# Performance work log

Measured on AMD Instinct MI355X. Metric: run time of the kernel, lower is better.

The kernel has to match this reference:

```python
import jax, jax.numpy as jnp
import numpy as np

LBASE = 256
L1_BASE = LBASE // 2 + 1   # 129
LPA = 128
L1_PA = LPA + 1            # 129
L2 = 16
L2_HALF = L2 // 2          # 8
L3 = 64
LOUTPUT = L3 + LPA + LBASE // 2  # 320
MAX_PLY = 60
COUNT = 6
BUCKET_SIZE = MAX_PLY // COUNT   # 10
B = 262144


def setup_inputs() -> dict:
    key = jax.random.key(0)
    ks = jax.random.split(key, 12)
    def w(k, shape, fan_in):
        bound = 1.0 / np.sqrt(fan_in)
        return jax.random.uniform(k, shape, jnp.float32, -bound, bound)
    return {
        "x_base": jax.random.uniform(ks[0], (B, LBASE // 2), jnp.float32),
        "x_pa": jax.random.uniform(ks[1], (B, LPA), jnp.float32),
        "mobility": jax.random.uniform(ks[2], (B, 1), jnp.float32),
        "ply": jax.random.randint(ks[3], (B,), 0, MAX_PLY),
        "W1b": w(ks[4], (COUNT, L2_HALF, L1_BASE), L1_BASE),
        "b1b": w(ks[5], (COUNT, L2_HALF), L1_BASE),
        "W1pa": w(ks[6], (COUNT, L2_HALF, L1_PA), L1_PA),
        "b1pa": w(ks[7], (COUNT, L2_HALF), L1_PA),
        "W2": w(ks[8], (COUNT, L3, L2 * 2), L2 * 2),
        "b2": w(ks[9], (COUNT, L3), L2 * 2),
        "Wout": w(ks[10], (COUNT, 1, LOUTPUT), LOUTPUT),
        "bout": jnp.zeros((COUNT, 1), jnp.float32),  # bias zeroed in __init__
    }


def _stacked_linear(x, W, b, idx):
    # per-sample bucket selection: x (B,I), W (C,O,I), b (C,O), idx (B,)
    return jnp.einsum("bi,boi->bo", x, W[idx]) + b[idx]


def reference(x_base, x_pa, mobility, ply, W1b, b1b, W1pa, b1pa, W2, b2, Wout, bout):
    idx = ply // BUCKET_SIZE                                   # (B,)
    mob = jnp.minimum(mobility * (7.0 / 255.0), 1.0)           # clamp max only
    xb = jnp.concatenate([x_base, mob], axis=1)                # (B,129)
    xpa = jnp.concatenate([x_pa, mob], axis=1)                 # (B,129)
    l1 = jnp.concatenate([
        _stacked_linear(xb, W1b, b1b, idx),
        _stacked_linear(xpa, W1pa, b1pa, idx),
    ], axis=1)                                                 # (B,16)
    l1_sq = jnp.square(l1) * (255.0 / 256.0)
    l1c = jnp.clip(jnp.concatenate([l1_sq, l1], axis=1), 0.0, 1.0)  # (B,32)
    l2x = _stacked_linear(l1c, W2, b2, idx)                    # (B,64)
    l2x = jnp.square(jnp.clip(l2x, 0.0, 1.0)) * (255.0 / 256.0)
    feats = jnp.concatenate([l2x, x_base, x_pa], axis=1)       # (B,320)
    return _stacked_linear(feats, Wout, bout, idx)             # (B,1)
```

## Files before the change

### kernel.cpp

```cpp
#include <hip/hip_runtime.h>


#define NB 6
#define BT 512
#define NW (BT / 64)

typedef _Float16 h2 __attribute__((ext_vector_type(2)));
typedef _Float16 h8 __attribute__((ext_vector_type(8)));
typedef float f4 __attribute__((ext_vector_type(4)));

__device__ __forceinline__ h2 pk2(float x, float y) {
    return __builtin_bit_cast(h2, __builtin_amdgcn_cvt_pkrtz(x, y));
}

__device__ __forceinline__ h8 pack8(const float4 a, const float4 b) {
    h2 p0 = pk2(a.x, a.y), p1 = pk2(a.z, a.w);
    h2 p2 = pk2(b.x, b.y), p3 = pk2(b.z, b.w);
    h8 r;
    r[0] = p0[0]; r[1] = p0[1]; r[2] = p1[0]; r[3] = p1[1];
    r[4] = p2[0]; r[5] = p2[1]; r[6] = p3[0]; r[7] = p3[1];
    return r;
}

__device__ __forceinline__ float actv(float v) {
    float u = fminf(fmaxf(v, 0.0f), 1.0f);
    return u * u * (255.0f / 256.0f);
}

__global__ __launch_bounds__(BT, 4)
void layerstacks_mfma(const float* __restrict__ x_base,
                      const float* __restrict__ x_pa,
                      const float* __restrict__ mobility,
                      const int*   __restrict__ ply,
                      const float* __restrict__ W1b,
                      const float* __restrict__ b1b,
                      const float* __restrict__ W1pa,
                      const float* __restrict__ b1pa,
                      const float* __restrict__ W2,
                      const float* __restrict__ b2,
                      const float* __restrict__ Wout,
                      const float* __restrict__ bout,
                      float* __restrict__ out)
{
    __shared__ __align__(16) _Float16 sW1[NB][2][4][4][9][8];
    __shared__ __align__(16) _Float16 sW2[NB][4][4][16][8];
    __shared__ float sWo0[NB][64];
    __shared__ float sB2[NB][64];
    __shared__ float sB1[NB][4][8];
    __shared__ float sBout[NB];
    __shared__ float sMob[BT];
    __shared__ int   sList[BT + NB * 16];
    __shared__ __align__(16) char sL1[NW * 1280];
    __shared__ int sCnt[8], sCur[8], sTb[40];
    __shared__ int sNt;

    const int tid   = threadIdx.x;
    const int lane  = tid & 63;
    const int w     = tid >> 6;
    const int gbase = blockIdx.x * BT;

    if (tid < 8) { sCnt[tid] = 0; }

    for (int e = tid; e < NB * 2 * 4 * 4 * 9 * 8; e += BT) {
        int i = e & 7;
        int rest = e >> 3;
        int n = rest % 9;   rest /= 9;
        int kb = rest & 3;  rest >>= 2;
        int t = rest & 3;   rest >>= 2;
        int st = rest & 1;
        int b = rest >> 1;
        int k = t * 32 + kb * 8 + i;
        float v;
        if (n < 8) {
            const float* Wx = st ? W1pa : W1b;
            v = Wx[b * 1032 + n * 129 + k];
        } else {
            v = st ? Wout[b * 320 + 192 + k] : Wout[b * 320 + 64 + k];
        }
        sW1[b][st][t][kb][n][i] = (_Float16)v;
    }
    for (int e = tid; e < NB * 4 * 4 * 16 * 8; e += BT) {
        int i = e & 7;
        int j = (e >> 3) & 15;
        int kb = (e >> 7) & 3;
        int T = (e >> 9) & 3;
        int b = e >> 11;
        int n = T * 16 + j;
        int k = kb * 8 + i;
        int u = k >> 1;
        int colw = (k & 1) ? (16 + u) : u;
        sW2[b][T][kb][j][i] = (_Float16)W2[b * 2048 + n * 32 + colw];
    }
    for (int e = tid; e < NB * 64; e += BT) {
        int b = e >> 6, n = e & 63;
        sWo0[b][n] = Wout[b * 320 + n];
        sB2[b][n]  = b2[e];
    }
    if (tid < NB * 4 * 8) {
        int n = tid & 7, which = (tid >> 3) & 3, b = tid >> 5;
        float v;
        if (which == 0)      v = b1b[b * 8 + n];
        else if (which == 1) v = b1pa[b * 8 + n];
        else if (which == 2) v = W1b [b * 1032 + n * 129 + 128];
        else                 v = W1pa[b * 1032 + n * 129 + 128];
        sB1[b][which][n] = v;
    }
    if (tid < NB) sBout[tid] = bout[tid];
    sMob[tid] = fminf(mobility[gbase + tid] * (7.0f / 255.0f), 1.0f);
    for (int e = tid; e < BT + NB * 16; e += BT) sList[e] = -1;

    const int bb = ply[gbase + tid] / 10;
    __syncthreads();

    #pragma unroll
    for (int b = 0; b < NB; ++b) {
        unsigned long long mk = __ballot(bb == b);
        if (bb == b) {
            int lead = __ffsll((long long)mk) - 1;
            if (lane == lead) atomicAdd(&sCnt[b], __popcll(mk));
        }
    }
    __syncthreads();

    if (tid == 0) {
        int off = 0, tt = 0;
        for (int b = 0; b < NB; ++b) {
            sCur[b] = off;
            int ntl = (sCnt[b] + 15) >> 4;
            for (int q = 0; q < ntl; ++q) sTb[tt++] = b;
            off += ntl << 4;
        }
        sNt = tt;
    }
    __syncthreads();

    #pragma unroll
    for (int b = 0; b < NB; ++b) {
        unsigned long long mk = __ballot(bb == b);
        if (bb == b) {
            int lead = __ffsll((long long)mk) - 1;
            int pfx = __popcll(mk & ((1ull << lane) - 1ull));
            int base = 0;
            if (lane == lead) base = atomicAdd(&sCur[b], __popcll(mk));
            base = __shfl(base, lead);
            sList[base + pfx] = tid;
        }
    }
    __syncthreads();

    const int ntiles = sNt;
    const int col = lane & 15;
    const int qd  = lane >> 4;
    char* lb = sL1 + w * 1280;

    for (int tl = w; tl < ntiles; tl += NW) {
        const int bkt = sTb[tl];
        const int t16 = tl << 4;

        const int sl0 = sList[t16 + qd * 4 + 0];
        const int sl1 = sList[t16 + qd * 4 + 1];
        const int sl2 = sList[t16 + qd * 4 + 2];
        const int sl3 = sList[t16 + qd * 4 + 3];
        int sA = sList[t16 + col];
        if (sA < 0) sA = sList[t16];

        const float* xbrow = x_base + (size_t)(gbase + sA) * 128 + qd * 8;
        const float* xprow = x_pa   + (size_t)(gbase + sA) * 128 + qd * 8;
        const float4 b00 = *(const float4*)(xbrow + 0);
        const float4 b01 = *(const float4*)(xbrow + 4);
        const float4 b10 = *(const float4*)(xbrow + 32);
        const float4 b11 = *(const float4*)(xbrow + 36);
        const float4 b20 = *(const float4*)(xbrow + 64);
        const float4 b21 = *(const float4*)(xbrow + 68);
        const float4 b30 = *(const float4*)(xbrow + 96);
        const float4 b31 = *(const float4*)(xbrow + 100);
        const float4 q00 = *(const float4*)(xprow + 0);
        const float4 q01 = *(const float4*)(xprow + 4);
        const float4 q10 = *(const float4*)(xprow + 32);
        const float4 q11 = *(const float4*)(xprow + 36);
        const float4 q20 = *(const float4*)(xprow + 64);
        const float4 q21 = *(const float4*)(xprow + 68);
        const float4 q30 = *(const float4*)(xprow + 96);
        const float4 q31 = *(const float4*)(xprow + 100);

        const float mob0 = (sl0 >= 0) ? sMob[sl0] : 0.0f;
        const float mob1 = (sl1 >= 0) ? sMob[sl1] : 0.0f;
        const float mob2 = (sl2 >= 0) ? sMob[sl2] : 0.0f;
        const float mob3 = (sl3 >= 0) ? sMob[sl3] : 0.0f;

        const int c7 = col & 7;
        const bool a8 = (col < 8);
        const int ncl = a8 ? col : 8;

        const h8 wa0 = *(const h8*)&sW1[bkt][0][0][qd][ncl][0];
        const h8 wa1 = *(const h8*)&sW1[bkt][0][1][qd][ncl][0];
        const h8 wa2 = *(const h8*)&sW1[bkt][0][2][qd][ncl][0];
        const h8 wa3 = *(const h8*)&sW1[bkt][0][3][qd][ncl][0];
        const h8 wp0 = *(const h8*)&sW1[bkt][1][0][qd][ncl][0];
        const h8 wp1 = *(const h8*)&sW1[bkt][1][1][qd][ncl][0];
        const h8 wp2 = *(const h8*)&sW1[bkt][1][2][qd][ncl][0];
        const h8 wp3 = *(const h8*)&sW1[bkt][1][3][qd][ncl][0];

        const float bb1 = sB1[bkt][0][c7], bp1 = sB1[bkt][1][c7];
        const float mwb = sB1[bkt][2][c7], mwp = sB1[bkt][3][c7];
        f4 cb, cp;
        cb[0] = a8 ? bb1 + mwb * mob0 : 0.0f;
        cb[1] = a8 ? bb1 + mwb * mob1 : 0.0f;
        cb[2] = a8 ? bb1 + mwb * mob2 : 0.0f;
        cb[3] = a8 ? bb1 + mwb * mob3 : 0.0f;
        cp[0] = a8 ? bp1 + mwp * mob0 : 0.0f;
        cp[1] = a8 ? bp1 + mwp * mob1 : 0.0f;
        cp[2] = a8 ? bp1 + mwp * mob2 : 0.0f;
        cp[3] = a8 ? bp1 + mwp * mob3 : 0.0f;

        cb = __builtin_amdgcn_mfma_f32_16x16x32_f16(pack8(b00, b01), wa0, cb, 0, 0, 0);
        cp = __builtin_amdgcn_mfma_f32_16x16x32_f16(pack8(q00, q01), wp0, cp, 0, 0, 0);
        cb = __builtin_amdgcn_mfma_f32_16x16x32_f16(pack8(b10, b11), wa1, cb, 0, 0, 0);
        cp = __builtin_amdgcn_mfma_f32_16x16x32_f16(pack8(q10, q11), wp1, cp, 0, 0, 0);
        cb = __builtin_amdgcn_mfma_f32_16x16x32_f16(pack8(b20, b21), wa2, cb, 0, 0, 0);
        cp = __builtin_amdgcn_mfma_f32_16x16x32_f16(pack8(q20, q21), wp2, cp, 0, 0, 0);
        cb = __builtin_amdgcn_mfma_f32_16x16x32_f16(pack8(b30, b31), wa3, cb, 0, 0, 0);
        cp = __builtin_amdgcn_mfma_f32_16x16x32_f16(pack8(q30, q31), wp3, cp, 0, 0, 0);

        if (col < 8) {
            #pragma unroll
            for (int r = 0; r < 4; ++r) {
                const int row = qd * 4 + r;
                float v = cb[r];
                *(h2*)(lb + row * 80 + col * 4) =
                    pk2(fminf(v * v * (255.0f / 256.0f), 1.0f),
                        fminf(fmaxf(v, 0.0f), 1.0f));
                v = cp[r];
                *(h2*)(lb + row * 80 + 32 + col * 4) =
                    pk2(fminf(v * v * (255.0f / 256.0f), 1.0f),
                        fminf(fmaxf(v, 0.0f), 1.0f));
            }
        } else if (col == 8) {
            #pragma unroll
            for (int r = 0; r < 4; ++r) {
                const int row = qd * 4 + r;
                *(float*)(lb + row * 80 + 64) = cb[r];
                *(float*)(lb + row * 80 + 68) = cp[r];
            }
        }

        const h8 a2 = *(const h8*)(lb + col * 80 + qd * 16);
        const float s0 = sB2[bkt][col];
        const float s1 = sB2[bkt][16 + col];
        const float s2 = sB2[bkt][32 + col];
        const float s3 = sB2[bkt][48 + col];
        f4 c20 = {s0, s0, s0, s0};
        f4 c21 = {s1, s1, s1, s1};
        f4 c22 = {s2, s2, s2, s2};
        f4 c23 = {s3, s3, s3, s3};
        c20 = __builtin_amdgcn_mfma_f32_16x16x32_f16(a2, *(const h8*)&sW2[bkt][0][qd][col][0], c20, 0, 0, 0);
        c21 = __builtin_amdgcn_mfma_f32_16x16x32_f16(a2, *(const h8*)&sW2[bkt][1][qd][col][0], c21, 0, 0, 0);
        c22 = __builtin_amdgcn_mfma_f32_16x16x32_f16(a2, *(const h8*)&sW2[bkt][2][qd][col][0], c22, 0, 0, 0);
        c23 = __builtin_amdgcn_mfma_f32_16x16x32_f16(a2, *(const h8*)&sW2[bkt][3][qd][col][0], c23, 0, 0, 0);

        const float wo0 = sWo0[bkt][col];
        const float wo1 = sWo0[bkt][16 + col];
        const float wo2 = sWo0[bkt][32 + col];
        const float wo3 = sWo0[bkt][48 + col];
        float p0 = actv(c20[0]) * wo0 + actv(c21[0]) * wo1 + actv(c22[0]) * wo2 + actv(c23[0]) * wo3;
        float p1 = actv(c20[1]) * wo0 + actv(c21[1]) * wo1 + actv(c22[1]) * wo2 + actv(c23[1]) * wo3;
        float p2 = actv(c20[2]) * wo0 + actv(c21[2]) * wo1 + actv(c22[2]) * wo2 + actv(c23[2]) * wo3;
        float p3 = actv(c20[3]) * wo0 + actv(c21[3]) * wo1 + actv(c22[3]) * wo2 + actv(c23[3]) * wo3;
        #pragma unroll
        for (int m = 1; m < 16; m <<= 1) {
            p0 += __shfl_xor(p0, m, 64);
            p1 += __shfl_xor(p1, m, 64);
            p2 += __shfl_xor(p2, m, 64);
            p3 += __shfl_xor(p3, m, 64);
        }

        if (col == 0) {
            const float bo = sBout[bkt];
            if (sl0 >= 0)
                out[gbase + sl0] = bo + *(const float*)(lb + (qd * 4 + 0) * 80 + 64)
                                      + *(const float*)(lb + (qd * 4 + 0) * 80 + 68) + p0;
            if (sl1 >= 0)
                out[gbase + sl1] = bo + *(const float*)(lb + (qd * 4 + 1) * 80 + 64)
                                      + *(const float*)(lb + (qd * 4 + 1) * 80 + 68) + p1;
            if (sl2 >= 0)
                out[gbase + sl2] = bo + *(const float*)(lb + (qd * 4 + 2) * 80 + 64)
                                      + *(const float*)(lb + (qd * 4 + 2) * 80 + 68) + p2;
            if (sl3 >= 0)
                out[gbase + sl3] = bo + *(const float*)(lb + (qd * 4 + 3) * 80 + 64)
                                      + *(const float*)(lb + (qd * 4 + 3) * 80 + 68) + p3;
        }
    }
}

extern "C" void kernel_launch(void* const* d_in, const int* in_sizes, int n_in,
                              void* d_out, int out_size, void* d_ws, size_t ws_size,
                              hipStream_t stream) {
    const float* x_base   = (const float*)d_in[0];
    const float* x_pa     = (const float*)d_in[1];
    const float* mobility = (const float*)d_in[2];
    const int*   ply      = (const int*)d_in[3];
    const float* W1b      = (const float*)d_in[4];
    const float* b1b      = (const float*)d_in[5];
    const float* W1pa     = (const float*)d_in[6];
    const float* b1pa     = (const float*)d_in[7];
    const float* W2       = (const float*)d_in[8];
    const float* b2       = (const float*)d_in[9];
    const float* Wout     = (const float*)d_in[10];
    const float* bout     = (const float*)d_in[11];
    float* out = (float*)d_out;

    const int B = in_sizes[3];
    const int blocks = B / BT;
    layerstacks_mfma<<<blocks, BT, 0, stream>>>(
        x_base, x_pa, mobility, ply, W1b, b1b, W1pa, b1pa, W2, b2, Wout, bout, out);
}
```

Before: 60.79 us.

## Pre-pack fp16 weights in a separate kernel and read them from global memory

Adds a small pre-pass kernel that converts W1/Wout/W2 into the fp16 MFMA-friendly layout in workspace once per call. The main kernel no longer stages these weights in LDS per block and loads the fragments directly from global (L2-cached) memory. This removes the redundant per-block repacking and the LDS footprint, and the launch bound is raised to 8 waves/SIMD-worth of blocks for higher occupancy. In exchange it adds a second kernel launch and turns the weight-fragment reads from LDS into global loads.

```diff
diff --git a/kernel.cpp b/kernel.cpp
--- a/kernel.cpp
+++ b/kernel.cpp
@@ -8,6 +8,9 @@
 typedef _Float16 h2 __attribute__((ext_vector_type(2)));
 typedef _Float16 h8 __attribute__((ext_vector_type(8)));
 typedef float f4 __attribute__((ext_vector_type(4)));
+
+#define GW1_ELEMS (NB * 2 * 4 * 4 * 9 * 8)
+#define GW2_ELEMS (NB * 4 * 4 * 16 * 8)
 
 __device__ __forceinline__ h2 pk2(float x, float y) {
     return __builtin_bit_cast(h2, __builtin_amdgcn_cvt_pkrtz(x, y));
@@ -27,23 +30,62 @@
     return u * u * (255.0f / 256.0f);
 }
 
-__global__ __launch_bounds__(BT, 4)
+__global__ __launch_bounds__(1024)
+void k_pack(const float* __restrict__ W1b, const float* __restrict__ W1pa,
+            const float* __restrict__ W2, const float* __restrict__ Wout,
+            _Float16* __restrict__ gW1, _Float16* __restrict__ gW2)
+{
+    const int i0 = blockIdx.x * 1024 + threadIdx.x;
+    const int stride = gridDim.x * 1024;
+
+    for (int e = i0; e < GW1_ELEMS; e += stride) {
+        int i = e & 7;
+        int rest = e >> 3;
+        int n = rest % 9;   rest /= 9;
+        int qd = rest & 3;  rest >>= 2;
+        int t = rest & 3;   rest >>= 2;
+        int st = rest & 1;
+        int b = rest >> 1;
+        int k = t * 32 + qd * 8 + i;
+        float v;
+        if (n < 8) {
+            const float* Wx = st ? W1pa : W1b;
+            v = Wx[b * 1032 + n * 129 + k];
+        } else {
+            v = st ? Wout[b * 320 + 192 + k] : Wout[b * 320 + 64 + k];
+        }
+        gW1[e] = (_Float16)v;
+    }
+    for (int e = i0; e < GW2_ELEMS; e += stride) {
+        int i = e & 7;
+        int j = (e >> 3) & 15;
+        int qd = (e >> 7) & 3;
+        int T = (e >> 9) & 3;
+        int b = e >> 11;
+        int n = T * 16 + j;
+        int k = qd * 8 + i;
+        int u = k >> 1;
+        int colw = (k & 1) ? (16 + u) : u;
+        gW2[e] = (_Float16)W2[b * 2048 + n * 32 + colw];
+    }
+}
+
+__global__ __launch_bounds__(BT, 8)
 void layerstacks_mfma(const float* __restrict__ x_base,
                       const float* __restrict__ x_pa,
                       const float* __restrict__ mobility,
                       const int*   __restrict__ ply,
+                      const float* __restrict__ b1b,
+                      const float* __restrict__ b1pa,
                       const float* __restrict__ W1b,
-                      const float* __restrict__ b1b,
                       const float* __restrict__ W1pa,
-                      const float* __restrict__ b1pa,
-                      const float* __restrict__ W2,
                       const float* __restrict__ b2,
                       const float* __restrict__ Wout,
                       const float* __restrict__ bout,
+                      const _Float16* __restrict__ gW1,
+                      const _Float16* __restrict__ gW2,
                       float* __restrict__ out)
 {
-    __shared__ __align__(16) _Float16 sW1[NB][2][4][4][9][8];
-    __shared__ __align__(16) _Float16 sW2[NB][4][4][16][8];
     __shared__ float sWo0[NB][64];
     __shared__ float sB2[NB][64];
     __shared__ float sB1[NB][4][8];
@@ -60,37 +102,6 @@
     const int gbase = blockIdx.x * BT;
 
     if (tid < 8) { sCnt[tid] = 0; }
-
-    for (int e = tid; e < NB * 2 * 4 * 4 * 9 * 8; e += BT) {
-        int i = e & 7;
-        int rest = e >> 3;
-        int n = rest % 9;   rest /= 9;
-        int kb = rest & 3;  rest >>= 2;
-        int t = rest & 3;   rest >>= 2;
-        int st = rest & 1;
-        int b = rest >> 1;
-        int k = t * 32 + kb * 8 + i;
-        float v;
-        if (n < 8) {
-            const float* Wx = st ? W1pa : W1b;
-            v = Wx[b * 1032 + n * 129 + k];
-        } else {
-            v = st ? Wout[b * 320 + 192 + k] : Wout[b * 320 + 64 + k];
-        }
-        sW1[b][st][t][kb][n][i] = (_Float16)v;
-    }
-    for (int e = tid; e < NB * 4 * 4 * 16 * 8; e += BT) {
-        int i = e & 7;
-        int j = (e >> 3) & 15;
-        int kb = (e >> 7) & 3;
-        int T = (e >> 9) & 3;
-        int b = e >> 11;
-        int n = T * 16 + j;
-        int k = kb * 8 + i;
-        int u = k >> 1;
-        int colw = (k & 1) ? (16 + u) : u;
-        sW2[b][T][kb][j][i] = (_Float16)W2[b * 2048 + n * 32 + colw];
-    }
     for (int e = tid; e < NB * 64; e += BT) {
         int b = e >> 6, n = e & 63;
         sWo0[b][n] = Wout[b * 320 + n];
@@ -192,14 +203,17 @@
         const bool a8 = (col < 8);
         const int ncl = a8 ? col : 8;
 
-        const h8 wa0 = *(const h8*)&sW1[bkt][0][0][qd][ncl][0];
-        const h8 wa1 = *(const h8*)&sW1[bkt][0][1][qd][ncl][0];
-        const h8 wa2 = *(const h8*)&sW1[bkt][0][2][qd][ncl][0];
-        const h8 wa3 = *(const h8*)&sW1[bkt][0][3][qd][ncl][0];
-        const h8 wp0 = *(const h8*)&sW1[bkt][1][0][qd][ncl][0];
-        const h8 wp1 = *(const h8*)&sW1[bkt][1][1][qd][ncl][0];
-        const h8 wp2 = *(const h8*)&sW1[bkt][1][2][qd][ncl][0];
-        const h8 wp3 = *(const h8*)&sW1[bkt][1][3][qd][ncl][0];
+        const _Float16* w1p = gW1 + (size_t)bkt * (2 * 4 * 4 * 9 * 8);
+        const _Float16* w1a = w1p + (size_t)qd * 72 + (size_t)ncl * 8;
+        const _Float16* w1q = w1a + (size_t)(4 * 4 * 9 * 8);
+        const h8 wa0 = *(const h8*)(w1a + 0 * 288);
+        const h8 wa1 = *(const h8*)(w1a + 1 * 288);
+        const h8 wa2 = *(const h8*)(w1a + 2 * 288);
+        const h8 wa3 = *(const h8*)(w1a + 3 * 288);
+        const h8 wp0 = *(const h8*)(w1q + 0 * 288);
+        const h8 wp1 = *(const h8*)(w1q + 1 * 288);
+        const h8 wp2 = *(const h8*)(w1q + 2 * 288);
+        const h8 wp3 = *(const h8*)(w1q + 3 * 288);
 
         const float bb1 = sB1[bkt][0][c7], bp1 = sB1[bkt][1][c7];
         const float mwb = sB1[bkt][2][c7], mwp = sB1[bkt][3][c7];
@@ -245,6 +259,8 @@
         }
 
         const h8 a2 = *(const h8*)(lb + col * 80 + qd * 16);
+        const _Float16* w2p = gW2 + (size_t)bkt * (4 * 4 * 16 * 8)
+                                  + (size_t)qd * 128 + (size_t)col * 8;
         const float s0 = sB2[bkt][col];
         const float s1 = sB2[bkt][16 + col];
         const float s2 = sB2[bkt][32 + col];
@@ -253,10 +269,10 @@
         f4 c21 = {s1, s1, s1, s1};
         f4 c22 = {s2, s2, s2, s2};
         f4 c23 = {s3, s3, s3, s3};
-        c20 = __builtin_amdgcn_mfma_f32_16x16x32_f16(a2, *(const h8*)&sW2[bkt][0][qd][col][0], c20, 0, 0, 0);
-        c21 = __builtin_amdgcn_mfma_f32_16x16x32_f16(a2, *(const h8*)&sW2[bkt][1][qd][col][0], c21, 0, 0, 0);
-        c22 = __builtin_amdgcn_mfma_f32_16x16x32_f16(a2, *(const h8*)&sW2[bkt][2][qd][col][0], c22, 0, 0, 0);
-        c23 = __builtin_amdgcn_mfma_f32_16x16x32_f16(a2, *(const h8*)&sW2[bkt][3][qd][col][0], c23, 0, 0, 0);
+        c20 = __builtin_amdgcn_mfma_f32_16x16x32_f16(a2, *(const h8*)(w2p + 0 * 512), c20, 0, 0, 0);
+        c21 = __builtin_amdgcn_mfma_f32_16x16x32_f16(a2, *(const h8*)(w2p + 1 * 512), c21, 0, 0, 0);
+        c22 = __builtin_amdgcn_mfma_f32_16x16x32_f16(a2, *(const h8*)(w2p + 2 * 512), c22, 0, 0, 0);
+        c23 = __builtin_amdgcn_mfma_f32_16x16x32_f16(a2, *(const h8*)(w2p + 3 * 512), c23, 0, 0, 0);
 
         const float wo0 = sWo0[bkt][col];
         const float wo1 = sWo0[bkt][16 + col];
@@ -309,8 +325,12 @@
     const float* bout     = (const float*)d_in[11];
     float* out = (float*)d_out;
 
+    _Float16* gW1 = (_Float16*)d_ws;
+    _Float16* gW2 = gW1 + GW1_ELEMS;
+
     const int B = in_sizes[3];
-    const int blocks = B / BT;
-    layerstacks_mfma<<<blocks, BT, 0, stream>>>(
-        x_base, x_pa, mobility, ply, W1b, b1b, W1pa, b1pa, W2, b2, Wout, bout, out);
-}
+    k_pack<<<16, 1024, 0, stream>>>(W1b, W1pa, W2, Wout, gW1, gW2);
+    layerstacks_mfma<<<B / BT, BT, 0, stream>>>(
+        x_base, x_pa, mobility, ply, b1b, b1pa, W1b, W1pa, b2, Wout, bout,
+        gW1, gW2, out);
+}
```

New measurement: 126.0 us. +107.3%, slower.
